# Optimization experiments

Measured on AMD Instinct MI355X. Metric: run time of the kernel, lower is better.

Reference implementation:

```python
import jax, jax.numpy as jnp
import numpy as np
import math

IN_DIM = 1024
OUT_DIM = 1024
GRID_SIZE = 5
SPLINE_ORDER = 3
N_COEFFS = GRID_SIZE + SPLINE_ORDER          # 8
N_KNOTS = GRID_SIZE + 2 * SPLINE_ORDER + 1   # 12
EPS = 1e-08


def setup_inputs() -> dict:
    key = jax.random.key(0)
    k_x, k_c, k_w = jax.random.split(key, 3)
    B = 4096
    x = jax.random.normal(k_x, (B, IN_DIM), dtype=jnp.float32)
    coeffs = jax.random.normal(k_c, (OUT_DIM, IN_DIM * N_COEFFS), dtype=jnp.float32) * 0.1
    # kaiming_uniform(a=sqrt(5)) -> U(-bound, bound), bound = sqrt(6/((1+a^2)*fan_in)) = 1/sqrt(fan_in)
    bound = 1.0 / math.sqrt(IN_DIM)
    base_weight = jax.random.uniform(k_w, (OUT_DIM, IN_DIM), dtype=jnp.float32,
                                     minval=-bound, maxval=bound)
    step = 2.0 / GRID_SIZE
    init_val = math.log(math.exp(step) - 1.0)
    grid_steps_log = jnp.full((IN_DIM, N_KNOTS - 1), init_val, dtype=jnp.float32)
    grid_start = jnp.full((IN_DIM, 1), -1.0 - SPLINE_ORDER * step, dtype=jnp.float32)
    res_scale = jnp.zeros((1,), dtype=jnp.float32)
    return {"x": x, "coeffs": coeffs, "base_weight": base_weight,
            "grid_steps_log": grid_steps_log, "grid_start": grid_start,
            "res_scale": res_scale}


def _get_grid(grid_steps_log, grid_start):
    steps = jax.nn.softplus(grid_steps_log)            # [in, n_knots-1]
    grid = jnp.concatenate([grid_start, steps], axis=-1)
    return jnp.cumsum(grid, axis=-1)                   # [in, n_knots]


def _b_spline(x, grid):
    # x: [B, in], grid: [in, n_knots] -> bases: [B, in, n_coeffs]
    x_u = x[:, :, None]                                # [B, in, 1]
    g = grid[None, :, :]                               # [1, in, n_knots]
    bases = ((x_u >= g[:, :, :-1]) & (x_u < g[:, :, 1:])).astype(x.dtype)
    for d in range(1, SPLINE_ORDER + 1):
        left = (x_u - g[:, :, :-(d + 1)]) / (g[:, :, d:-1] - g[:, :, :-(d + 1)] + EPS)
        right = (g[:, :, d + 1:] - x_u) / (g[:, :, d + 1:] - g[:, :, 1:-d] + EPS)
        bases = left * bases[:, :, :-1] + right * bases[:, :, 1:]
    return bases


def reference(x, coeffs, base_weight, grid_steps_log, grid_start, res_scale):
    grid = _get_grid(grid_steps_log, grid_start)
    spline_basis = _b_spline(x, grid)                  # [B, in, n_coeffs]
    B = spline_basis.shape[0]
    spline_flat = spline_basis.reshape(B, -1)          # [B, in*n_coeffs]
    spline_out = spline_flat @ coeffs.T                # [B, out]
    base_out = jax.nn.silu(x) @ base_weight.T          # [B, out]
    y = spline_out + base_out
    y = y + res_scale * x                              # residual (in_dim == out_dim)
    return y
```

## Files before the change

### kernel.cpp

```cpp
#include <hip/hip_runtime.h>

#define IN_DIM   1024
#define OUT_DIM  1024
#define BATCH    4096
#define NC       8
#define NK       12
#define KSPLINE  (IN_DIM * NC)
#define KDIM     (KSPLINE + IN_DIM)
#define EPS      1e-8f
#define KSPLIT   4
#define KT_PER   (KDIM / 64 / KSPLIT)

typedef _Float16 f16x8 __attribute__((ext_vector_type(8)));
typedef float    f32x4 __attribute__((ext_vector_type(4)));

static __device__ __forceinline__ unsigned short f2h_bits(float f) {
  _Float16 h = (_Float16)f;
  return __builtin_bit_cast(unsigned short, h);
}

static __device__ __forceinline__ void gl_lds16(const unsigned short* g, unsigned short* l) {
  __builtin_amdgcn_global_load_lds(
      (const __attribute__((address_space(1))) unsigned int*)g,
      (__attribute__((address_space(3))) unsigned int*)l, 16, 0, 0);
}

__global__ void build_grid_k(const float* __restrict__ gsl,
                             const float* __restrict__ gstart,
                             float* __restrict__ gT,
                             float* __restrict__ rT) {
  int i = blockIdx.x * 256 + threadIdx.x;
  if (i >= IN_DIM) return;
  float g[NK];
  float acc = gstart[i];
  g[0] = acc;
#pragma unroll
  for (int t = 0; t < NK - 1; ++t) {
    float v  = gsl[i * (NK - 1) + t];
    float sp = (v > 20.f) ? v : log1pf(expf(v));
    acc += sp;
    g[t + 1] = acc;
  }
#pragma unroll
  for (int t = 0; t < NK; ++t) gT[t * IN_DIM + i] = g[t];
#pragma unroll
  for (int j = 0; j < 11; ++j) rT[(j)      * IN_DIM + i] = 1.f / (g[j + 1] - g[j] + EPS);
#pragma unroll
  for (int j = 0; j < 10; ++j) rT[(11 + j) * IN_DIM + i] = 1.f / (g[j + 2] - g[j] + EPS);
#pragma unroll
  for (int j = 0; j <  9; ++j) rT[(21 + j) * IN_DIM + i] = 1.f / (g[j + 3] - g[j] + EPS);
}

__global__ __launch_bounds__(256, 2) void build_A_k(const float* __restrict__ x,
                                                    const float* __restrict__ gT,
                                                    const float* __restrict__ rT,
                                                    const float* __restrict__ rsp,
                                                    unsigned short* __restrict__ A,
                                                    float* __restrict__ out) {
  const int i  = (blockIdx.x & 3) * 256 + threadIdx.x;
  const int b0 = (blockIdx.x >> 2) * 16;
  const float rs = rsp[0];
  float g[NK], r[30];
#pragma unroll
  for (int t = 0; t < NK; ++t) g[t] = gT[t * IN_DIM + i];
#pragma unroll
  for (int t = 0; t < 30; ++t) r[t] = rT[t * IN_DIM + i];

  for (int bb = 0; bb < 16; ++bb) {
    const int b = b0 + bb;
    float xv = x[(size_t)b * IN_DIM + i];
    float bas[NK - 1];
#pragma unroll
    for (int k = 0; k < NK - 1; ++k)
      bas[k] = (xv >= g[k] && xv < g[k + 1]) ? 1.f : 0.f;
    const int off[3] = {0, 11, 21};
#pragma unroll
    for (int d = 1; d <= 3; ++d) {
#pragma unroll
      for (int k = 0; k < NK - 1 - d; ++k) {
        float left  = (xv - g[k])         * r[off[d - 1] + k];
        float right = (g[k + d + 1] - xv) * r[off[d - 1] + k + 1];
        bas[k] = left * bas[k] + right * bas[k + 1];
      }
    }
    uint4 pack;
    pack.x = (unsigned)f2h_bits(bas[0]) | ((unsigned)f2h_bits(bas[1]) << 16);
    pack.y = (unsigned)f2h_bits(bas[2]) | ((unsigned)f2h_bits(bas[3]) << 16);
    pack.z = (unsigned)f2h_bits(bas[4]) | ((unsigned)f2h_bits(bas[5]) << 16);
    pack.w = (unsigned)f2h_bits(bas[6]) | ((unsigned)f2h_bits(bas[7]) << 16);
    *(uint4*)&A[(size_t)b * KDIM + i * NC] = pack;
    float s = xv / (1.f + expf(-xv));
    A[(size_t)b * KDIM + KSPLINE + i] = f2h_bits(s);
    out[(size_t)b * OUT_DIM + i] = rs * xv;
  }
}

__global__ void build_W_k(const float* __restrict__ coeffs,
                          const float* __restrict__ bw,
                          unsigned short* __restrict__ W) {
  int idx = blockIdx.x * 256 + threadIdx.x;
  int n  = idx / (KDIM / 4);
  int k4 = (idx - n * (KDIM / 4)) * 4;
  float4 v;
  if (k4 < KSPLINE) v = *(const float4*)&coeffs[(size_t)n * KSPLINE + k4];
  else              v = *(const float4*)&bw[(size_t)n * IN_DIM + (k4 - KSPLINE)];
  ushort4 o;
  o.x = f2h_bits(v.x); o.y = f2h_bits(v.y); o.z = f2h_bits(v.z); o.w = f2h_bits(v.w);
  *(ushort4*)&W[(size_t)n * KDIM + k4] = o;
}

__global__ __launch_bounds__(256) void gemm_k(const unsigned short* __restrict__ A,
                                              const unsigned short* __restrict__ W,
                                              float* __restrict__ out) {
  __shared__ __align__(16) unsigned short As[128 * 64];
  __shared__ __align__(16) unsigned short Bs[128 * 64];
  const int tid  = threadIdx.x;
  const int wave = tid >> 6;
  const int lane = tid & 63;
  const int ks = blockIdx.x >> 8;
  const int t  = blockIdx.x & 255;
  const int bm = t & 31;
  const int bn = t >> 5;
  const int l3 = lane >> 3;
  const int l7 = lane & 7;
  const int colsw = (l7 ^ l3) * 8;
  const unsigned short* aG = A + (size_t)(bm * 128 + wave * 8 + l3) * KDIM + colsw
                               + (size_t)ks * (KT_PER * 64);
  const unsigned short* bG = W + (size_t)(bn * 128 + wave * 8 + l3) * KDIM + colsw
                               + (size_t)ks * (KT_PER * 64);

  f32x4 acc[4][4] = {};
  const int quad = lane >> 4;
  const int r16  = lane & 15;
  const int wm   = (wave >> 1) * 64;
  const int wn   = (wave & 1) * 64;

  for (int kt = 0; kt < KT_PER; ++kt) {
    __syncthreads();
#pragma unroll
    for (int j = 0; j < 4; ++j) {
      gl_lds16(aG + (size_t)j * 32 * KDIM, &As[(j * 4 + wave) * 512]);
      gl_lds16(bG + (size_t)j * 32 * KDIM, &Bs[(j * 4 + wave) * 512]);
    }
    __syncthreads();
#pragma unroll
    for (int kk = 0; kk < 2; ++kk) {
      f16x8 af[4], bf[4];
#pragma unroll
      for (int mt = 0; mt < 4; ++mt) {
        int row = wm + mt * 16 + r16;
        int col = (kk * 32 + quad * 8) ^ ((row & 7) * 8);
        af[mt] = *(const f16x8*)&As[row * 64 + col];
      }
#pragma unroll
      for (int nt = 0; nt < 4; ++nt) {
        int row = wn + nt * 16 + r16;
        int col = (kk * 32 + quad * 8) ^ ((row & 7) * 8);
        bf[nt] = *(const f16x8*)&Bs[row * 64 + col];
      }
#pragma unroll
      for (int mt = 0; mt < 4; ++mt)
#pragma unroll
        for (int nt = 0; nt < 4; ++nt)
          acc[mt][nt] = __builtin_amdgcn_mfma_f32_16x16x32_f16(af[mt], bf[nt], acc[mt][nt], 0, 0, 0);
    }
    aG += 64;
    bG += 64;
  }

#pragma unroll
  for (int mt = 0; mt < 4; ++mt) {
#pragma unroll
    for (int r = 0; r < 4; ++r) {
      int row = bm * 128 + wm + mt * 16 + quad * 4 + r;
      float* orow = out + (size_t)row * OUT_DIM;
#pragma unroll
      for (int nt = 0; nt < 4; ++nt) {
        int col = bn * 128 + wn + nt * 16 + r16;
        atomicAdd(&orow[col], acc[mt][nt][r]);
      }
    }
  }
}

extern "C" void kernel_launch(void* const* d_in, const int* in_sizes, int n_in,
                              void* d_out, int out_size, void* d_ws, size_t ws_size,
                              hipStream_t stream) {
  const float* x      = (const float*)d_in[0];
  const float* coeffs = (const float*)d_in[1];
  const float* bw     = (const float*)d_in[2];
  const float* gsl    = (const float*)d_in[3];
  const float* gstart = (const float*)d_in[4];
  const float* rsp    = (const float*)d_in[5];

  char* ws = (char*)d_ws;
  unsigned short* A  = (unsigned short*)ws;
  unsigned short* W  = (unsigned short*)(ws + (size_t)BATCH * KDIM * 2);
  float*          gT = (float*)W;
  float*          rT = gT + 12 * IN_DIM;
  float*          out = (float*)d_out;

  build_grid_k<<<4, 256, 0, stream>>>(gsl, gstart, gT, rT);
  build_A_k<<<(IN_DIM / 256) * (BATCH / 16), 256, 0, stream>>>(x, gT, rT, rsp, A, out);
  build_W_k<<<(OUT_DIM * (KDIM / 4)) / 256, 256, 0, stream>>>(coeffs, bw, W);
  gemm_k<<<256 * KSPLIT, 256, 0, stream>>>(A, W, out);
}
```

Before: 260.6 us.

## Fuse grid, A-build and W-build kernels into one prep kernel

Merges the grid-construction, spline-basis/A-matrix build and weight-conversion kernels into a single launch. Each A-block recomputes its own grid knots and reciprocals from the raw parameters instead of reading precomputed tables, and W-conversion blocks are appended after the A blocks in the same grid. This removes two kernel launches and their serialization gaps, and lets A and W conversion overlap, at the cost of redundant per-block softplus and reciprocal work and the loss of the two-blocks-per-CU launch bound on the A path.

```diff
diff --git a/kernel.cpp b/kernel.cpp
--- a/kernel.cpp
+++ b/kernel.cpp
@@ -10,6 +10,9 @@
 #define EPS      1e-8f
 #define KSPLIT   4
 #define KT_PER   (KDIM / 64 / KSPLIT)
+
+#define NBLK_A   ((IN_DIM / 256) * (BATCH / 16))
+#define NBLK_W   ((OUT_DIM * (KDIM / 4)) / 256)
 
 typedef _Float16 f16x8 __attribute__((ext_vector_type(8)));
 typedef float    f32x4 __attribute__((ext_vector_type(4)));
@@ -25,88 +28,76 @@
       (__attribute__((address_space(3))) unsigned int*)l, 16, 0, 0);
 }
 
-__global__ void build_grid_k(const float* __restrict__ gsl,
-                             const float* __restrict__ gstart,
-                             float* __restrict__ gT,
-                             float* __restrict__ rT) {
-  int i = blockIdx.x * 256 + threadIdx.x;
-  if (i >= IN_DIM) return;
-  float g[NK];
-  float acc = gstart[i];
-  g[0] = acc;
+__global__ __launch_bounds__(256) void prep_k(const float* __restrict__ x,
+                                              const float* __restrict__ coeffs,
+                                              const float* __restrict__ bw,
+                                              const float* __restrict__ gsl,
+                                              const float* __restrict__ gstart,
+                                              const float* __restrict__ rsp,
+                                              unsigned short* __restrict__ A,
+                                              unsigned short* __restrict__ W,
+                                              float* __restrict__ out) {
+  const int blk = blockIdx.x;
+  if (blk < NBLK_A) {
+    const int i  = (blk & 3) * 256 + threadIdx.x;
+    const int b0 = (blk >> 2) * 16;
+    const float rs = rsp[0];
+    float g[NK];
+    float acc = gstart[i];
+    g[0] = acc;
 #pragma unroll
-  for (int t = 0; t < NK - 1; ++t) {
-    float v  = gsl[i * (NK - 1) + t];
-    float sp = (v > 20.f) ? v : log1pf(expf(v));
-    acc += sp;
-    g[t + 1] = acc;
+    for (int t = 0; t < NK - 1; ++t) {
+      float v  = gsl[i * (NK - 1) + t];
+      float sp = (v > 20.f) ? v : log1pf(expf(v));
+      acc += sp;
+      g[t + 1] = acc;
+    }
+    float r[30];
+#pragma unroll
+    for (int j = 0; j < 11; ++j) r[j]      = 1.f / (g[j + 1] - g[j] + EPS);
+#pragma unroll
+    for (int j = 0; j < 10; ++j) r[11 + j] = 1.f / (g[j + 2] - g[j] + EPS);
+#pragma unroll
+    for (int j = 0; j <  9; ++j) r[21 + j] = 1.f / (g[j + 3] - g[j] + EPS);
+
+    for (int bb = 0; bb < 16; ++bb) {
+      const int b = b0 + bb;
+      float xv = x[(size_t)b * IN_DIM + i];
+      float bas[NK - 1];
+#pragma unroll
+      for (int k = 0; k < NK - 1; ++k)
+        bas[k] = (xv >= g[k] && xv < g[k + 1]) ? 1.f : 0.f;
+      const int off[3] = {0, 11, 21};
+#pragma unroll
+      for (int d = 1; d <= 3; ++d) {
+#pragma unroll
+        for (int k = 0; k < NK - 1 - d; ++k) {
+          float left  = (xv - g[k])         * r[off[d - 1] + k];
+          float right = (g[k + d + 1] - xv) * r[off[d - 1] + k + 1];
+          bas[k] = left * bas[k] + right * bas[k + 1];
+        }
+      }
+      uint4 pack;
+      pack.x = (unsigned)f2h_bits(bas[0]) | ((unsigned)f2h_bits(bas[1]) << 16);
+      pack.y = (unsigned)f2h_bits(bas[2]) | ((unsigned)f2h_bits(bas[3]) << 16);
+      pack.z = (unsigned)f2h_bits(bas[4]) | ((unsigned)f2h_bits(bas[5]) << 16);
+      pack.w = (unsigned)f2h_bits(bas[6]) | ((unsigned)f2h_bits(bas[7]) << 16);
+      *(uint4*)&A[(size_t)b * KDIM + i * NC] = pack;
+      float s = xv / (1.f + expf(-xv));
+      A[(size_t)b * KDIM + KSPLINE + i] = f2h_bits(s);
+      out[(size_t)b * OUT_DIM + i] = rs * xv;
+    }
+  } else {
+    int idx = (blk - NBLK_A) * 256 + threadIdx.x;
+    int n  = idx / (KDIM / 4);
+    int k4 = (idx - n * (KDIM / 4)) * 4;
+    float4 v;
+    if (k4 < KSPLINE) v = *(const float4*)&coeffs[(size_t)n * KSPLINE + k4];
+    else              v = *(const float4*)&bw[(size_t)n * IN_DIM + (k4 - KSPLINE)];
+    ushort4 o;
+    o.x = f2h_bits(v.x); o.y = f2h_bits(v.y); o.z = f2h_bits(v.z); o.w = f2h_bits(v.w);
+    *(ushort4*)&W[(size_t)n * KDIM + k4] = o;
   }
-#pragma unroll
-  for (int t = 0; t < NK; ++t) gT[t * IN_DIM + i] = g[t];
-#pragma unroll
-  for (int j = 0; j < 11; ++j) rT[(j)      * IN_DIM + i] = 1.f / (g[j + 1] - g[j] + EPS);
-#pragma unroll
-  for (int j = 0; j < 10; ++j) rT[(11 + j) * IN_DIM + i] = 1.f / (g[j + 2] - g[j] + EPS);
-#pragma unroll
-  for (int j = 0; j <  9; ++j) rT[(21 + j) * IN_DIM + i] = 1.f / (g[j + 3] - g[j] + EPS);
-}
-
-__global__ __launch_bounds__(256, 2) void build_A_k(const float* __restrict__ x,
-                                                    const float* __restrict__ gT,
-                                                    const float* __restrict__ rT,
-                                                    const float* __restrict__ rsp,
-                                                    unsigned short* __restrict__ A,
-                                                    float* __restrict__ out) {
-  const int i  = (blockIdx.x & 3) * 256 + threadIdx.x;
-  const int b0 = (blockIdx.x >> 2) * 16;
-  const float rs = rsp[0];
-  float g[NK], r[30];
-#pragma unroll
-  for (int t = 0; t < NK; ++t) g[t] = gT[t * IN_DIM + i];
-#pragma unroll
-  for (int t = 0; t < 30; ++t) r[t] = rT[t * IN_DIM + i];
-
-  for (int bb = 0; bb < 16; ++bb) {
-    const int b = b0 + bb;
-    float xv = x[(size_t)b * IN_DIM + i];
-    float bas[NK - 1];
-#pragma unroll
-    for (int k = 0; k < NK - 1; ++k)
-      bas[k] = (xv >= g[k] && xv < g[k + 1]) ? 1.f : 0.f;
-    const int off[3] = {0, 11, 21};
-#pragma unroll
-    for (int d = 1; d <= 3; ++d) {
-#pragma unroll
-      for (int k = 0; k < NK - 1 - d; ++k) {
-        float left  = (xv - g[k])         * r[off[d - 1] + k];
-        float right = (g[k + d + 1] - xv) * r[off[d - 1] + k + 1];
-        bas[k] = left * bas[k] + right * bas[k + 1];
-      }
-    }
-    uint4 pack;
-    pack.x = (unsigned)f2h_bits(bas[0]) | ((unsigned)f2h_bits(bas[1]) << 16);
-    pack.y = (unsigned)f2h_bits(bas[2]) | ((unsigned)f2h_bits(bas[3]) << 16);
-    pack.z = (unsigned)f2h_bits(bas[4]) | ((unsigned)f2h_bits(bas[5]) << 16);
-    pack.w = (unsigned)f2h_bits(bas[6]) | ((unsigned)f2h_bits(bas[7]) << 16);
-    *(uint4*)&A[(size_t)b * KDIM + i * NC] = pack;
-    float s = xv / (1.f + expf(-xv));
-    A[(size_t)b * KDIM + KSPLINE + i] = f2h_bits(s);
-    out[(size_t)b * OUT_DIM + i] = rs * xv;
-  }
-}
-
-__global__ void build_W_k(const float* __restrict__ coeffs,
-                          const float* __restrict__ bw,
-                          unsigned short* __restrict__ W) {
-  int idx = blockIdx.x * 256 + threadIdx.x;
-  int n  = idx / (KDIM / 4);
-  int k4 = (idx - n * (KDIM / 4)) * 4;
-  float4 v;
-  if (k4 < KSPLINE) v = *(const float4*)&coeffs[(size_t)n * KSPLINE + k4];
-  else              v = *(const float4*)&bw[(size_t)n * IN_DIM + (k4 - KSPLINE)];
-  ushort4 o;
-  o.x = f2h_bits(v.x); o.y = f2h_bits(v.y); o.z = f2h_bits(v.z); o.w = f2h_bits(v.w);
-  *(ushort4*)&W[(size_t)n * KDIM + k4] = o;
 }
 
 __global__ __launch_bounds__(256) void gemm_k(const unsigned short* __restrict__ A,
@@ -196,12 +187,8 @@
   char* ws = (char*)d_ws;
   unsigned short* A  = (unsigned short*)ws;
   unsigned short* W  = (unsigned short*)(ws + (size_t)BATCH * KDIM * 2);
-  float*          gT = (float*)W;
-  float*          rT = gT + 12 * IN_DIM;
   float*          out = (float*)d_out;
 
-  build_grid_k<<<4, 256, 0, stream>>>(gsl, gstart, gT, rT);
-  build_A_k<<<(IN_DIM / 256) * (BATCH / 16), 256, 0, stream>>>(x, gT, rT, rsp, A, out);
-  build_W_k<<<(OUT_DIM * (KDIM / 4)) / 256, 256, 0, stream>>>(coeffs, bw, W);
+  prep_k<<<NBLK_A + NBLK_W, 256, 0, stream>>>(x, coeffs, bw, gsl, gstart, rsp, A, W, out);
   gemm_k<<<256 * KSPLIT, 256, 0, stream>>>(A, W, out);
 }
```

After: 253.7 us. 1.03x faster.
